# Kernel tuning notes

Measured on AMD Instinct MI355X. Metric: run time of the kernel, lower is better.

Reference implementation:

```python
import jax, jax.numpy as jnp
import numpy as np
from jax import lax

NEG_SLOPE = 0.2
BN_EPS = 1e-5


def _edges(n_nodes, n_total):
    # complete graph (no self loops) on the first n_nodes nodes, as in create_complete_graph,
    # plus PyG GATConv default add_self_loops over ALL n_total nodes.
    i = np.arange(n_nodes)
    src = np.repeat(i, n_nodes)
    dst = np.tile(i, n_nodes)
    keep = src != dst
    loops = np.arange(n_total)
    src = np.concatenate([src[keep], loops]).astype(np.int32)
    dst = np.concatenate([dst[keep], loops]).astype(np.int32)
    return jnp.asarray(src), jnp.asarray(dst)


def _bn_eval(x, g, b, m, v):
    # x: [B, C, H, W]; eval-mode batchnorm with running stats
    inv = g / jnp.sqrt(v + BN_EPS)
    return x * inv[None, :, None, None] + (b - m * inv)[None, :, None, None]


def _gat(x, W, a_src, a_dst, bias, src, dst, n_total):
    h = x @ W                      # [N, D_out]
    s = h @ a_src                  # [N] per-node source score
    d = h @ a_dst                  # [N] per-node dest score
    e = jax.nn.leaky_relu(s[src] + d[dst], NEG_SLOPE)          # [E]
    emax = jax.ops.segment_max(e, dst, num_segments=n_total)   # [N]
    ex = jnp.exp(e - emax[dst])
    denom = jax.ops.segment_sum(ex, dst, num_segments=n_total)
    alpha = ex / denom[dst]                                    # [E]
    out = jax.ops.segment_sum(alpha[:, None] * h[src], dst, num_segments=n_total)
    return out + bias


def setup_inputs() -> dict:
    key = jax.random.key(0)
    ks = jax.random.split(key, 12)
    B, H, W = 8, 64, 64

    def rn(k, shape, s):
        return jax.random.normal(k, shape, jnp.float32) * s

    return {
        "images": jax.random.normal(ks[0], (B, 3, H, W), jnp.float32),
        "conv1_w": rn(ks[1], (64, 3, 3, 3), 0.1), "conv1_b": jnp.zeros((64,), jnp.float32),
        "bn1_g": jnp.ones((64,), jnp.float32), "bn1_b": jnp.zeros((64,), jnp.float32),
        "bn1_m": jnp.zeros((64,), jnp.float32), "bn1_v": jnp.ones((64,), jnp.float32),
        "conv2_w": rn(ks[2], (128, 64, 3, 3), 0.05), "conv2_b": jnp.zeros((128,), jnp.float32),
        "bn2_g": jnp.ones((128,), jnp.float32), "bn2_b": jnp.zeros((128,), jnp.float32),
        "bn2_m": jnp.zeros((128,), jnp.float32), "bn2_v": jnp.ones((128,), jnp.float32),
        "gat1_w": rn(ks[3], (128, 256), 0.05), "gat1_asrc": rn(ks[4], (256,), 0.05),
        "gat1_adst": rn(ks[5], (256,), 0.05), "gat1_bias": jnp.zeros((256,), jnp.float32),
        "gat2_w": rn(ks[6], (256, 128), 0.05), "gat2_asrc": rn(ks[7], (128,), 0.05),
        "gat2_adst": rn(ks[8], (128,), 0.05), "gat2_bias": jnp.zeros((128,), jnp.float32),
        "out_w": rn(ks[9], (128, 10), 0.05), "out_b": jnp.zeros((10,), jnp.float32),
    }


def reference(images, conv1_w, conv1_b, bn1_g, bn1_b, bn1_m, bn1_v,
              conv2_w, conv2_b, bn2_g, bn2_b, bn2_m, bn2_v,
              gat1_w, gat1_asrc, gat1_adst, gat1_bias,
              gat2_w, gat2_asrc, gat2_adst, gat2_bias,
              out_w, out_b):
    dn = ("NCHW", "OIHW", "NCHW")
    x = lax.conv_general_dilated(images, conv1_w, (1, 1), "SAME", dimension_numbers=dn)
    x = x + conv1_b[None, :, None, None]
    x = jax.nn.relu(_bn_eval(x, bn1_g, bn1_b, bn1_m, bn1_v))
    x = lax.reduce_window(x, -jnp.inf, lax.max, (1, 1, 2, 2), (1, 1, 2, 2), "VALID")
    x = lax.conv_general_dilated(x, conv2_w, (1, 1), "SAME", dimension_numbers=dn)
    x = x + conv2_b[None, :, None, None]
    x = jax.nn.relu(_bn_eval(x, bn2_g, bn2_b, bn2_m, bn2_v))

    B = x.shape[0]
    n_nodes = x.shape[2] * x.shape[3]          # (H/2)*(W/2) = 1024
    x = x.reshape(B, 128, n_nodes).transpose(0, 2, 1).reshape(-1, 128)  # [B*n, 128]
    n_total = B * n_nodes
    src, dst = _edges(n_nodes, n_total)

    x = jax.nn.relu(_gat(x, gat1_w, gat1_asrc, gat1_adst, gat1_bias, src, dst, n_total))
    x = jax.nn.relu(_gat(x, gat2_w, gat2_asrc, gat2_adst, gat2_bias, src, dst, n_total))

    x = x.reshape(B, n_nodes, 128).mean(axis=1)   # global_mean_pool over each image's nodes
    logits = x @ out_w + out_b
    return jax.nn.log_softmax(logits, axis=1)
```

## Files before the change

kernel.cpp:

```cpp
#include <hip/hip_runtime.h>
#include <math.h>

#define BN_EPS 1e-5f
#define NEG_SLOPE 0.2f

__device__ __forceinline__ float relu_f(float x) { return x > 0.f ? x : 0.f; }
__device__ __forceinline__ float leaky_f(float z) { return z > 0.f ? z : NEG_SLOPE * z; }

__global__ void conv1_pool(const float* __restrict__ img, const float* __restrict__ w,
                           const float* __restrict__ cb, const float* __restrict__ g,
                           const float* __restrict__ bb, const float* __restrict__ m,
                           const float* __restrict__ vv, float* __restrict__ out)
{
    int blk = blockIdx.x;
    int q = blk & 3, cog = (blk >> 2) & 15, b = blk >> 6;
    int t = threadIdx.x;
    int x = t & 31, y = (q << 3) + (t >> 5);

    float acc[4][4] = {};
#pragma unroll
    for (int ci = 0; ci < 3; ++ci) {
        const float* ib = img + (b * 3 + ci) * 4096;
        float rv[4][4];
#pragma unroll
        for (int r = 0; r < 4; ++r) {
            int yy = 2 * y - 1 + r;
            bool yok = (unsigned)yy < 64u;
            const float* p = ib + yy * 64 + 2 * x;
            float2 c01 = yok ? *(const float2*)p : make_float2(0.f, 0.f);
            rv[r][1] = c01.x;
            rv[r][2] = c01.y;
            rv[r][0] = (yok && x > 0) ? p[-1] : 0.f;
            rv[r][3] = (yok && x < 31) ? p[2] : 0.f;
        }
#pragma unroll
        for (int j = 0; j < 4; ++j) {
            const float* wj = w + ((cog * 4 + j) * 3 + ci) * 9;
#pragma unroll
            for (int ky = 0; ky < 3; ++ky)
#pragma unroll
                for (int kx = 0; kx < 3; ++kx) {
                    float wvv = wj[ky * 3 + kx];
#pragma unroll
                    for (int py = 0; py < 2; ++py)
#pragma unroll
                        for (int px = 0; px < 2; ++px)
                            acc[j][py * 2 + px] += rv[py + ky][px + kx] * wvv;
                }
        }
    }
#pragma unroll
    for (int j = 0; j < 4; ++j) {
        int co = cog * 4 + j;
        float inv = g[co] / sqrtf(vv[co] + BN_EPS);
        float sh = cb[co] * inv + (bb[co] - m[co] * inv);
        float v0 = relu_f(acc[j][0] * inv + sh);
        float v1 = relu_f(acc[j][1] * inv + sh);
        float v2 = relu_f(acc[j][2] * inv + sh);
        float v3 = relu_f(acc[j][3] * inv + sh);
        out[((b * 64 + co) * 32 + y) * 32 + x] = fmaxf(fmaxf(v0, v1), fmaxf(v2, v3));
    }
}

__global__ void conv2_split(const float* __restrict__ in, const float* __restrict__ w,
                            float* __restrict__ c2p)
{
    int blk = blockIdx.x;
    int kz = blk & 1, half = (blk >> 1) & 1, cog = (blk >> 2) & 31, b = blk >> 7;
    int t = threadIdx.x;
    int x2p = (t & 15) * 2;
    int y = half * 16 + (t >> 4);
    bool xnz = x2p != 0;
    bool xhi = x2p == 30;
    const float* ibase = in + b * 65536 + kz * 32768;
    int xb = xnz ? x2p - 1 : 0;

    float acc[4][2] = {};

#pragma unroll 2
    for (int ci = 0; ci < 32; ++ci) {
        const float* cb2 = ibase + ci * 1024;
        float rc[3][4];
#pragma unroll
        for (int r = 0; r < 3; ++r) {
            int yy = y - 1 + r;
            bool yok = (unsigned)yy < 32u;
            const float* p = cb2 + yy * 32 + xb;
            float4 f = yok ? *(const float4*)p : make_float4(0.f, 0.f, 0.f, 0.f);
            rc[r][0] = xnz ? f.x : 0.f;
            rc[r][1] = xnz ? f.y : f.x;
            rc[r][2] = xnz ? f.z : f.y;
            float r3 = xnz ? f.w : f.z;
            rc[r][3] = xhi ? 0.f : r3;
        }
#pragma unroll
        for (int j = 0; j < 4; ++j) {
            const float* wj = w + ((cog * 4 + j) * 64 + kz * 32 + ci) * 9;
#pragma unroll
            for (int ky = 0; ky < 3; ++ky)
#pragma unroll
                for (int kx = 0; kx < 3; ++kx) {
                    float wvv = wj[ky * 3 + kx];
                    acc[j][0] += rc[ky][kx] * wvv;
                    acc[j][1] += rc[ky][kx + 1] * wvv;
                }
        }
    }

    float* pp = c2p + (size_t)kz * 1048576;
    int bid = b * 64 + cog * 2 + half;
    size_t base = ((size_t)bid * 256 + t) * 8;
    float4 s0 = {acc[0][0], acc[1][0], acc[2][0], acc[3][0]};
    float4 s1 = {acc[0][1], acc[1][1], acc[2][1], acc[3][1]};
    *(float4*)&pp[base] = s0;
    *(float4*)&pp[base + 4] = s1;
}

__global__ void gemm1_conv(const float* __restrict__ c2p,
                           const float* __restrict__ cb, const float* __restrict__ g,
                           const float* __restrict__ bb, const float* __restrict__ mbn,
                           const float* __restrict__ vv,
                           const float* __restrict__ B, float* __restrict__ C,
                           const float* __restrict__ asrc, const float* __restrict__ adst,
                           float* __restrict__ sp, float* __restrict__ dp)
{
    __shared__ float As[16][33];
    __shared__ float Bs[16][64];
    __shared__ float invs[128];
    __shared__ float shs[128];
    int t = threadIdx.x;
    if (t < 128) {
        float iv = g[t] / sqrtf(vv[t] + BN_EPS);
        invs[t] = iv;
        shs[t] = cb[t] * iv + (bb[t] - mbn[t] * iv);
    }

    int m0 = blockIdx.x * 32;
    int n0 = blockIdx.y * 64;
    int tx = t & 15, ty = t >> 4;
    int am = t >> 3, ak2 = (t & 7) * 2;
    int mm = m0 + am;
    int b = mm >> 10, rem = mm & 1023, y = rem >> 5, x = rem & 31;
    int xp = x >> 1, odd = x & 1, half = y >> 4, yy = y & 15;
    int toff = yy * 16 + xp;
    size_t cbase = ((size_t)((b * 64 + half) * 256 + toff)) * 8 + odd * 4 + (ak2 & 3)
                 + (size_t)(ak2 >> 2) * 4096;
    const float* p0 = c2p + cbase;
    const float* p1 = c2p + 1048576 + cbase;
    __syncthreads();

    float acc[2][4] = {};
    for (int k0 = 0; k0 < 128; k0 += 16) {
        int k = k0 + ak2;
        float2 u = *(const float2*)&p0[(size_t)k0 * 1024];
        float2 w2 = *(const float2*)&p1[(size_t)k0 * 1024];
        float2 av;
        av.x = relu_f((u.x + w2.x) * invs[k] + shs[k]);
        av.y = relu_f((u.y + w2.y) * invs[k + 1] + shs[k + 1]);
        float4 bv = *(const float4*)&B[(size_t)(k0 + ty) * 256 + n0 + tx * 4];
        __syncthreads();
        As[ak2][am] = av.x;
        As[ak2 + 1][am] = av.y;
        *(float4*)&Bs[ty][tx * 4] = bv;
        __syncthreads();
#pragma unroll
        for (int kk = 0; kk < 16; ++kk) {
            float a0 = As[kk][ty * 2], a1 = As[kk][ty * 2 + 1];
            float4 b4 = *(const float4*)&Bs[kk][tx * 4];
            acc[0][0] += a0 * b4.x; acc[0][1] += a0 * b4.y;
            acc[0][2] += a0 * b4.z; acc[0][3] += a0 * b4.w;
            acc[1][0] += a1 * b4.x; acc[1][1] += a1 * b4.y;
            acc[1][2] += a1 * b4.z; acc[1][3] += a1 * b4.w;
        }
    }
#pragma unroll
    for (int i = 0; i < 2; ++i) {
        float4 o = {acc[i][0], acc[i][1], acc[i][2], acc[i][3]};
        *(float4*)&C[(size_t)(m0 + ty * 2 + i) * 256 + n0 + tx * 4] = o;
    }

    if (m0 < 1024) {
        float4 as4 = *(const float4*)&asrc[n0 + tx * 4];
        float4 ad4 = *(const float4*)&adst[n0 + tx * 4];
#pragma unroll
        for (int i = 0; i < 2; ++i) {
            float ss = acc[i][0] * as4.x + acc[i][1] * as4.y +
                       acc[i][2] * as4.z + acc[i][3] * as4.w;
            float dd = acc[i][0] * ad4.x + acc[i][1] * ad4.y +
                       acc[i][2] * ad4.z + acc[i][3] * ad4.w;
#pragma unroll
            for (int off = 1; off < 16; off <<= 1) {
                ss += __shfl_xor(ss, off);
                dd += __shfl_xor(dd, off);
            }
            if (tx == 0) {
                sp[blockIdx.y * 1024 + m0 + ty * 2 + i] = ss;
                dp[blockIdx.y * 1024 + m0 + ty * 2 + i] = dd;
            }
        }
    }
}

__global__ void gemm2_fused(const float* __restrict__ pacc1, const float* __restrict__ pden1,
                            const float* __restrict__ b1, const float* __restrict__ h1,
                            const float* __restrict__ B, float* __restrict__ C,
                            const float* __restrict__ asrc, const float* __restrict__ adst,
                            float* __restrict__ sp, float* __restrict__ dp)
{
    __shared__ float As[16][33];
    __shared__ float Bs[16][64];
    int t = threadIdx.x;
    int m0 = blockIdx.x * 32;
    int n0 = blockIdx.y * 64;
    int tx = t & 15, ty = t >> 4;
    int am = t >> 3, ak2 = (t & 7) * 2;
    int mm = m0 + am;
    bool lo = m0 < 1024;

    float rden = 0.f;
    const float* ap;
    if (lo) {
        float den = 0.f;
#pragma unroll
        for (int ks = 0; ks < 8; ++ks) den += pden1[ks * 1024 + mm];
        rden = 1.f / den;
        ap = pacc1 + (size_t)mm * 256 + ak2;
    } else {
        ap = h1 + (size_t)mm * 256 + ak2;
    }

    float acc[2][4] = {};
    for (int k0 = 0; k0 < 256; k0 += 16) {
        float2 av;
        float z0 = b1[k0 + ak2], z1 = b1[k0 + ak2 + 1];
        if (lo) {
            float sx = 0.f, sy = 0.f;
#pragma unroll
            for (int ks = 0; ks < 8; ++ks) {
                float2 u = *(const float2*)&ap[(size_t)ks * 262144 + k0];
                sx += u.x; sy += u.y;
            }
            av.x = relu_f(sx * rden + z0);
            av.y = relu_f(sy * rden + z1);
        } else {
            float2 u = *(const float2*)&ap[k0];
            av.x = relu_f(u.x + z0);
            av.y = relu_f(u.y + z1);
        }
        float4 bv = *(const float4*)&B[(size_t)(k0 + ty) * 128 + n0 + tx * 4];
        __syncthreads();
        As[ak2][am] = av.x;
        As[ak2 + 1][am] = av.y;
        *(float4*)&Bs[ty][tx * 4] = bv;
        __syncthreads();
#pragma unroll
        for (int kk = 0; kk < 16; ++kk) {
            float a0 = As[kk][ty * 2], a1 = As[kk][ty * 2 + 1];
            float4 b4 = *(const float4*)&Bs[kk][tx * 4];
            acc[0][0] += a0 * b4.x; acc[0][1] += a0 * b4.y;
            acc[0][2] += a0 * b4.z; acc[0][3] += a0 * b4.w;
            acc[1][0] += a1 * b4.x; acc[1][1] += a1 * b4.y;
            acc[1][2] += a1 * b4.z; acc[1][3] += a1 * b4.w;
        }
    }
#pragma unroll
    for (int i = 0; i < 2; ++i) {
        float4 o = {acc[i][0], acc[i][1], acc[i][2], acc[i][3]};
        *(float4*)&C[(size_t)(m0 + ty * 2 + i) * 128 + n0 + tx * 4] = o;
    }

    if (lo) {
        float4 as4 = *(const float4*)&asrc[n0 + tx * 4];
        float4 ad4 = *(const float4*)&adst[n0 + tx * 4];
#pragma unroll
        for (int i = 0; i < 2; ++i) {
            float ss = acc[i][0] * as4.x + acc[i][1] * as4.y +
                       acc[i][2] * as4.z + acc[i][3] * as4.w;
            float dd = acc[i][0] * ad4.x + acc[i][1] * ad4.y +
                       acc[i][2] * ad4.z + acc[i][3] * ad4.w;
#pragma unroll
            for (int off = 1; off < 16; off <<= 1) {
                ss += __shfl_xor(ss, off);
                dd += __shfl_xor(dd, off);
            }
            if (tx == 0) {
                sp[blockIdx.y * 1024 + m0 + ty * 2 + i] = ss;
                dp[blockIdx.y * 1024 + m0 + ty * 2 + i] = dd;
            }
        }
    }
}

template <int D, int KS, int NT>
__global__ void gat_agg_gemm(const float* __restrict__ h, const float* __restrict__ sp,
                             const float* __restrict__ dp, float* __restrict__ pacc,
                             float* __restrict__ pden)
{
    __shared__ float Ss[1024];
    __shared__ float As[16][33];
    __shared__ float Bs[16][64];
    __shared__ float red[4];
    __shared__ float part[16][32];

    const int CH = 1024 / KS;
    int t = threadIdx.x;
    int m0 = blockIdx.x * 32;
    int n0 = blockIdx.y * 64;
    int kz = blockIdx.z;
    int tx = t & 15, ty = t >> 4;
    int vg2 = tx * 2;

    float4 sa = {0.f, 0.f, 0.f, 0.f};
#pragma unroll
    for (int nt = 0; nt < NT; ++nt) {
        float4 u = *(const float4*)&sp[nt * 1024 + t * 4];
        sa.x += u.x; sa.y += u.y; sa.z += u.z; sa.w += u.w;
    }
    *(float4*)&Ss[t * 4] = sa;
    float lm = fmaxf(fmaxf(sa.x, sa.y), fmaxf(sa.z, sa.w));
#pragma unroll
    for (int off = 1; off < 64; off <<= 1) lm = fmaxf(lm, __shfl_xor(lm, off));
    if ((t & 63) == 0) red[t >> 6] = lm;
    __syncthreads();
    float smax = fmaxf(fmaxf(red[0], red[1]), fmaxf(red[2], red[3]));

    float dv0 = 0.f, dv1 = 0.f;
#pragma unroll
    for (int nt = 0; nt < NT; ++nt) {
        dv0 += dp[nt * 1024 + m0 + vg2];
        dv1 += dp[nt * 1024 + m0 + vg2 + 1];
    }
    float mv0 = leaky_f(smax + dv0), mv1 = leaky_f(smax + dv1);
    float ds0 = 0.f, ds1 = 0.f;
    float acc[2][4] = {};

    for (int k0 = kz * CH; k0 < kz * CH + CH; k0 += 16) {
        float4 bv = *(const float4*)&h[(size_t)(k0 + ty) * D + n0 + tx * 4];
        float su = Ss[k0 + ty];
        float a0 = __expf(leaky_f(su + dv0) - mv0);
        float a1 = __expf(leaky_f(su + dv1) - mv1);
        ds0 += a0; ds1 += a1;
        __syncthreads();
        As[ty][vg2] = a0;
        As[ty][vg2 + 1] = a1;
        *(float4*)&Bs[ty][tx * 4] = bv;
        __syncthreads();
#pragma unroll
        for (int kk = 0; kk < 16; ++kk) {
            float a0m = As[kk][ty * 2], a1m = As[kk][ty * 2 + 1];
            float4 b4 = *(const float4*)&Bs[kk][tx * 4];
            acc[0][0] += a0m * b4.x; acc[0][1] += a0m * b4.y;
            acc[0][2] += a0m * b4.z; acc[0][3] += a0m * b4.w;
            acc[1][0] += a1m * b4.x; acc[1][1] += a1m * b4.y;
            acc[1][2] += a1m * b4.z; acc[1][3] += a1m * b4.w;
        }
    }

    __syncthreads();
    part[ty][vg2] = ds0;
    part[ty][vg2 + 1] = ds1;
    __syncthreads();

#pragma unroll
    for (int i = 0; i < 2; ++i) {
        float4 o = {acc[i][0], acc[i][1], acc[i][2], acc[i][3]};
        *(float4*)&pacc[((size_t)kz * 1024 + m0 + ty * 2 + i) * D + n0 + tx * 4] = o;
    }
    if (t < 32) {
        float den = 0.f;
#pragma unroll
        for (int u = 0; u < 16; ++u) den += part[u][t];
        pden[kz * 1024 + m0 + t] = den;
    }
}

__global__ void pool_combine(const float* __restrict__ pacc2, const float* __restrict__ pden2,
                             const float* __restrict__ h2, const float* __restrict__ b2,
                             float* __restrict__ part)
{
    __shared__ float dinv[64];
    int blk = blockIdx.x;
    int b = blk >> 4, seg = blk & 15, t = threadIdx.x;
    float bz = b2[t];
    float acc = 0.f;
    if (b == 0) {
        if (t < 64) {
            int v = seg * 64 + t;
            float den = 0.f;
#pragma unroll
            for (int ks = 0; ks < 16; ++ks) den += pden2[ks * 1024 + v];
            dinv[t] = 1.f / den;
        }
        __syncthreads();
        for (int n = 0; n < 64; ++n) {
            int v = seg * 64 + n;
            float s = 0.f;
#pragma unroll
            for (int ks = 0; ks < 16; ++ks)
                s += pacc2[(size_t)(ks * 1024 + v) * 128 + t];
            acc += relu_f(s * dinv[n] + bz);
        }
    } else {
        const float* p = h2 + ((size_t)b * 1024 + seg * 64) * 128 + t;
#pragma unroll 8
        for (int n = 0; n < 64; ++n) acc += relu_f(p[(size_t)n * 128] + bz);
    }
    part[(b * 16 + seg) * 128 + t] = acc;
}

__global__ void head_kernel(const float* __restrict__ part, const float* __restrict__ ow,
                            const float* __restrict__ ob, float* __restrict__ out)
{
    __shared__ float pooled[128];
    __shared__ float logits[10];
    int b = blockIdx.x, t = threadIdx.x;
    float acc = 0.f;
#pragma unroll
    for (int sgi = 0; sgi < 16; ++sgi) acc += part[(b * 16 + sgi) * 128 + t];
    pooled[t] = acc * (1.f / 1024.f);
    __syncthreads();
    if (t < 10) {
        float l = ob[t];
        for (int c = 0; c < 128; ++c) l += pooled[c] * ow[c * 10 + t];
        logits[t] = l;
    }
    __syncthreads();
    if (t == 0) {
        float mx = logits[0];
        for (int j = 1; j < 10; ++j) mx = fmaxf(mx, logits[j]);
        float sum = 0.f;
        for (int j = 0; j < 10; ++j) sum += expf(logits[j] - mx);
        float lse = mx + logf(sum);
        for (int j = 0; j < 10; ++j) out[b * 10 + j] = logits[j] - lse;
    }
}

extern "C" void kernel_launch(void* const* d_in, const int* in_sizes, int n_in,
                              void* d_out, int out_size, void* d_ws, size_t ws_size,
                              hipStream_t stream)
{
    const float* images = (const float*)d_in[0];
    const float* c1w = (const float*)d_in[1];
    const float* c1b = (const float*)d_in[2];
    const float* bn1g = (const float*)d_in[3];
    const float* bn1b = (const float*)d_in[4];
    const float* bn1m = (const float*)d_in[5];
    const float* bn1v = (const float*)d_in[6];
    const float* c2w = (const float*)d_in[7];
    const float* c2b = (const float*)d_in[8];
    const float* bn2g = (const float*)d_in[9];
    const float* bn2b = (const float*)d_in[10];
    const float* bn2m = (const float*)d_in[11];
    const float* bn2v = (const float*)d_in[12];
    const float* g1w = (const float*)d_in[13];
    const float* g1as = (const float*)d_in[14];
    const float* g1ad = (const float*)d_in[15];
    const float* g1b = (const float*)d_in[16];
    const float* g2w = (const float*)d_in[17];
    const float* g2as = (const float*)d_in[18];
    const float* g2ad = (const float*)d_in[19];
    const float* g2b = (const float*)d_in[20];
    const float* ow = (const float*)d_in[21];
    const float* ob = (const float*)d_in[22];
    float* out = (float*)d_out;

    float* ws = (float*)d_ws;
    float* c2p   = ws;
    float* pacc1 = ws;
    float* h1    = ws + 2097152;
    float* pacc2 = ws + 2097152;
    float* bufc1 = ws + 4194304;
    float* h2    = ws + 4194304;
    float* sp1   = ws + 5242880;
    float* dp1   = ws + 5246976;
    float* sp2   = ws + 5251072;
    float* dp2   = ws + 5253120;
    float* pden1 = ws + 5255168;
    float* pden2 = ws + 5263360;
    float* part  = ws + 5279744;

    conv1_pool<<<512, 256, 0, stream>>>(images, c1w, c1b, bn1g, bn1b, bn1m, bn1v, bufc1);
    conv2_split<<<1024, 256, 0, stream>>>(bufc1, c2w, c2p);

    gemm1_conv<<<dim3(256, 4), 256, 0, stream>>>(
        c2p, c2b, bn2g, bn2b, bn2m, bn2v, g1w, h1, g1as, g1ad, sp1, dp1);
    gat_agg_gemm<256, 8, 4><<<dim3(32, 4, 8), 256, 0, stream>>>(h1, sp1, dp1, pacc1, pden1);

    gemm2_fused<<<dim3(256, 2), 256, 0, stream>>>(
        pacc1, pden1, g1b, h1, g2w, h2, g2as, g2ad, sp2, dp2);
    gat_agg_gemm<128, 16, 2><<<dim3(32, 2, 16), 256, 0, stream>>>(h2, sp2, dp2, pacc2, pden2);

    pool_combine<<<128, 128, 0, stream>>>(pacc2, pden2, h2, g2b, part);
    head_kernel<<<8, 128, 0, stream>>>(part, ow, ob, out);
}
```

Measured before the change: 235.1 us.

## Split conv2 combine into separate kernel and halve GAT aggregation K-splits

Adds a conv2_combine kernel that sums the two conv2 partial buffers, applies BN and ReLU, and writes a node-major [N,128] activation. gemm1 can then read A with simple contiguous loads instead of strided gathers. The split-K factor of both GAT aggregation kernels is halved (8→4 and 16→8), so the later reductions read fewer partial buffers. The workspace layout is reshuffled so buffers alias safely. The cost is an extra kernel launch plus a round trip of the activation through memory, and fewer blocks in the aggregation kernels.

```diff
diff --git a/kernel.cpp b/kernel.cpp
--- a/kernel.cpp
+++ b/kernel.cpp
@@ -116,47 +116,64 @@
     *(float4*)&pp[base + 4] = s1;
 }
 
-__global__ void gemm1_conv(const float* __restrict__ c2p,
-                           const float* __restrict__ cb, const float* __restrict__ g,
-                           const float* __restrict__ bb, const float* __restrict__ mbn,
-                           const float* __restrict__ vv,
-                           const float* __restrict__ B, float* __restrict__ C,
-                           const float* __restrict__ asrc, const float* __restrict__ adst,
-                           float* __restrict__ sp, float* __restrict__ dp)
+__global__ void conv2_combine(const float* __restrict__ c2p,
+                              const float* __restrict__ cb, const float* __restrict__ g,
+                              const float* __restrict__ bb, const float* __restrict__ m,
+                              const float* __restrict__ vv, float* __restrict__ x0)
+{
+    int gid = blockIdx.x * 256 + threadIdx.x;
+    int t = gid & 255, bid = gid >> 8;
+    int half = bid & 1, cog = (bid >> 1) & 31, b = bid >> 6;
+    size_t off = (size_t)gid * 8;
+
+    float4 u0 = *(const float4*)&c2p[off];
+    float4 u1 = *(const float4*)&c2p[off + 4];
+    float4 w0 = *(const float4*)&c2p[1048576 + off];
+    float4 w1 = *(const float4*)&c2p[1048576 + off + 4];
+    float sx = u0.x + w0.x, sy = u0.y + w0.y, sz = u0.z + w0.z, sw = u0.w + w0.w;
+    float qx = u1.x + w1.x, qy = u1.y + w1.y, qz = u1.z + w1.z, qw = u1.w + w1.w;
+
+    float4 gg = ((const float4*)g)[cog];
+    float4 vvv = ((const float4*)vv)[cog];
+    float4 bbb = ((const float4*)bb)[cog];
+    float4 mm = ((const float4*)m)[cog];
+    float4 cbb = ((const float4*)cb)[cog];
+    float ix = gg.x / sqrtf(vvv.x + BN_EPS);
+    float iy = gg.y / sqrtf(vvv.y + BN_EPS);
+    float iz = gg.z / sqrtf(vvv.z + BN_EPS);
+    float iw = gg.w / sqrtf(vvv.w + BN_EPS);
+    float shx = cbb.x * ix + (bbb.x - mm.x * ix);
+    float shy = cbb.y * iy + (bbb.y - mm.y * iy);
+    float shz = cbb.z * iz + (bbb.z - mm.z * iz);
+    float shw = cbb.w * iw + (bbb.w - mm.w * iw);
+
+    float4 o0 = {relu_f(sx * ix + shx), relu_f(sy * iy + shy),
+                 relu_f(sz * iz + shz), relu_f(sw * iw + shw)};
+    float4 o1 = {relu_f(qx * ix + shx), relu_f(qy * iy + shy),
+                 relu_f(qz * iz + shz), relu_f(qw * iw + shw)};
+
+    int y = half * 16 + (t >> 4), x2p = (t & 15) * 2;
+    int n0 = b * 1024 + y * 32 + x2p;
+    *(float4*)&x0[(size_t)n0 * 128 + cog * 4] = o0;
+    *(float4*)&x0[(size_t)(n0 + 1) * 128 + cog * 4] = o1;
+}
+
+__global__ void gemm1_k(const float* __restrict__ A, const float* __restrict__ B,
+                        float* __restrict__ C,
+                        const float* __restrict__ asrc, const float* __restrict__ adst,
+                        float* __restrict__ sp, float* __restrict__ dp)
 {
     __shared__ float As[16][33];
     __shared__ float Bs[16][64];
-    __shared__ float invs[128];
-    __shared__ float shs[128];
     int t = threadIdx.x;
-    if (t < 128) {
-        float iv = g[t] / sqrtf(vv[t] + BN_EPS);
-        invs[t] = iv;
-        shs[t] = cb[t] * iv + (bb[t] - mbn[t] * iv);
-    }
-
     int m0 = blockIdx.x * 32;
     int n0 = blockIdx.y * 64;
     int tx = t & 15, ty = t >> 4;
     int am = t >> 3, ak2 = (t & 7) * 2;
-    int mm = m0 + am;
-    int b = mm >> 10, rem = mm & 1023, y = rem >> 5, x = rem & 31;
-    int xp = x >> 1, odd = x & 1, half = y >> 4, yy = y & 15;
-    int toff = yy * 16 + xp;
-    size_t cbase = ((size_t)((b * 64 + half) * 256 + toff)) * 8 + odd * 4 + (ak2 & 3)
-                 + (size_t)(ak2 >> 2) * 4096;
-    const float* p0 = c2p + cbase;
-    const float* p1 = c2p + 1048576 + cbase;
-    __syncthreads();
-
     float acc[2][4] = {};
+
     for (int k0 = 0; k0 < 128; k0 += 16) {
-        int k = k0 + ak2;
-        float2 u = *(const float2*)&p0[(size_t)k0 * 1024];
-        float2 w2 = *(const float2*)&p1[(size_t)k0 * 1024];
-        float2 av;
-        av.x = relu_f((u.x + w2.x) * invs[k] + shs[k]);
-        av.y = relu_f((u.y + w2.y) * invs[k + 1] + shs[k + 1]);
+        float2 av = *(const float2*)&A[(size_t)(m0 + am) * 128 + k0 + ak2];
         float4 bv = *(const float4*)&B[(size_t)(k0 + ty) * 256 + n0 + tx * 4];
         __syncthreads();
         As[ak2][am] = av.x;
@@ -222,7 +239,7 @@
     if (lo) {
         float den = 0.f;
 #pragma unroll
-        for (int ks = 0; ks < 8; ++ks) den += pden1[ks * 1024 + mm];
+        for (int ks = 0; ks < 4; ++ks) den += pden1[ks * 1024 + mm];
         rden = 1.f / den;
         ap = pacc1 + (size_t)mm * 256 + ak2;
     } else {
@@ -236,7 +253,7 @@
         if (lo) {
             float sx = 0.f, sy = 0.f;
 #pragma unroll
-            for (int ks = 0; ks < 8; ++ks) {
+            for (int ks = 0; ks < 4; ++ks) {
                 float2 u = *(const float2*)&ap[(size_t)ks * 262144 + k0];
                 sx += u.x; sy += u.y;
             }
@@ -388,15 +405,16 @@
             int v = seg * 64 + t;
             float den = 0.f;
 #pragma unroll
-            for (int ks = 0; ks < 16; ++ks) den += pden2[ks * 1024 + v];
+            for (int ks = 0; ks < 8; ++ks) den += pden2[ks * 1024 + v];
             dinv[t] = 1.f / den;
         }
         __syncthreads();
+#pragma unroll 2
         for (int n = 0; n < 64; ++n) {
             int v = seg * 64 + n;
             float s = 0.f;
 #pragma unroll
-            for (int ks = 0; ks < 16; ++ks)
+            for (int ks = 0; ks < 8; ++ks)
                 s += pacc2[(size_t)(ks * 1024 + v) * 128 + t];
             acc += relu_f(s * dinv[n] + bz);
         }
@@ -466,29 +484,30 @@
 
     float* ws = (float*)d_ws;
     float* c2p   = ws;
-    float* pacc1 = ws;
-    float* h1    = ws + 2097152;
-    float* pacc2 = ws + 2097152;
-    float* bufc1 = ws + 4194304;
-    float* h2    = ws + 4194304;
-    float* sp1   = ws + 5242880;
-    float* dp1   = ws + 5246976;
-    float* sp2   = ws + 5251072;
-    float* dp2   = ws + 5253120;
-    float* pden1 = ws + 5255168;
-    float* pden2 = ws + 5263360;
-    float* part  = ws + 5279744;
+    float* bufc1 = ws + 2097152;
+    float* h1    = ws + 2621440;
+    float* x0    = ws + 4718592;
+    float* h2    = ws + 5767168;
+    float* sp1   = ws + 6815744;
+    float* dp1   = ws + 6819840;
+    float* sp2   = ws + 6823936;
+    float* dp2   = ws + 6825984;
+    float* part  = bufc1;
+    float* pden1 = bufc1 + 16384;
+    float* pden2 = bufc1 + 24576;
+    float* pacc1 = x0;
+    float* pacc2 = h1;
 
     conv1_pool<<<512, 256, 0, stream>>>(images, c1w, c1b, bn1g, bn1b, bn1m, bn1v, bufc1);
     conv2_split<<<1024, 256, 0, stream>>>(bufc1, c2w, c2p);
-
-    gemm1_conv<<<dim3(256, 4), 256, 0, stream>>>(
-        c2p, c2b, bn2g, bn2b, bn2m, bn2v, g1w, h1, g1as, g1ad, sp1, dp1);
-    gat_agg_gemm<256, 8, 4><<<dim3(32, 4, 8), 256, 0, stream>>>(h1, sp1, dp1, pacc1, pden1);
+    conv2_combine<<<512, 256, 0, stream>>>(c2p, c2b, bn2g, bn2b, bn2m, bn2v, x0);
+
+    gemm1_k<<<dim3(256, 4), 256, 0, stream>>>(x0, g1w, h1, g1as, g1ad, sp1, dp1);
+    gat_agg_gemm<256, 4, 4><<<dim3(32, 4, 4), 256, 0, stream>>>(h1, sp1, dp1, pacc1, pden1);
 
     gemm2_fused<<<dim3(256, 2), 256, 0, stream>>>(
         pacc1, pden1, g1b, h1, g2w, h2, g2as, g2ad, sp2, dp2);
-    gat_agg_gemm<128, 16, 2><<<dim3(32, 2, 16), 256, 0, stream>>>(h2, sp2, dp2, pacc2, pden2);
+    gat_agg_gemm<128, 8, 2><<<dim3(32, 2, 8), 256, 0, stream>>>(h2, sp2, dp2, pacc2, pden2);
 
     pool_combine<<<128, 128, 0, stream>>>(pacc2, pden2, h2, g2b, part);
     head_kernel<<<8, 128, 0, stream>>>(part, ow, ob, out);
```

Measured after the change: 219.7 us. -6.5%, faster.
